# Performance work log

Measured on AMD Instinct MI355X. Metric: run time of the kernel, lower is better.

Reference implementation:

```python
import jax, jax.numpy as jnp
import numpy as np

# ---- layer_param constants (ihmehimmeli alpha-synapse defaults, see shape_source) ----
K_NO_SPIKE = 1000.0
DECAY_RATE = 1.0          # K in exp(K*t)
DECAY_RATE_INV = 1.0
FIRE_THRESHOLD = 1.0
IN_FEATURES = 1024
OUT_FEATURES = 512
N_PULSE = 10
BATCH = 32
MIN_W_ARG = -0.3678794411714423  # -1/e, domain boundary of Lambert W0


def lambertw0(x):
    """Principal branch Lambert W on [-1/e, 0], via Halley iterations."""
    e = jnp.exp(1.0)
    # series init near the branch point, w ~= x for small |x|
    w = jnp.where(x < -0.25,
                  -1.0 + jnp.sqrt(jnp.maximum(2.0 * (1.0 + e * x), 0.0)),
                  x * (1.0 - x))
    def halley(w, _):
        ew = jnp.exp(w)
        f = w * ew - x
        denom = ew * (w + 1.0) - (w + 2.0) * f / (2.0 * (w + 1.0) + 1e-12)
        w = w - f / (denom + 1e-12)
        return w, None
    w, _ = jax.lax.scan(halley, w, None, length=12)
    return w


def _alpha_solve(act, weight):
    """Causal-set cumulative spike-time solve for alpha synapses.
    act: [B,N] input spike times, weight: [O,N].
    V(t) = e^{-K t} (A t - B) with A = sum w e^{K t_i}, B = sum w t_i e^{K t_i};
    threshold crossing: t* = B/A - W0(-theta*K/A * e^{K B/A})/K,
    valid if t* lies between the last included and the next input spike.
    """
    order = jnp.argsort(act, axis=1)                             # [B,N]
    t_s = jnp.take_along_axis(act, order, axis=1)                # sorted spike times
    valid_in = t_s < K_NO_SPIKE
    z = jnp.where(valid_in, jnp.exp(DECAY_RATE * t_s), 0.0)      # exp of valid sorted spikes
    w_s = weight[:, order].transpose(1, 0, 2)                    # [B,O,N] weights in sorted order
    A_c = jnp.cumsum(w_s * z[:, None, :], axis=2)                # causal-set cumulative A
    B_c = jnp.cumsum(w_s * (z * t_s)[:, None, :], axis=2)        # causal-set cumulative B
    A_pos = A_c > 1e-10
    A_safe = jnp.where(A_pos, A_c, 1.0)
    b_over_a = B_c / A_safe
    arg = -FIRE_THRESHOLD * DECAY_RATE / A_safe * jnp.exp(jnp.minimum(DECAY_RATE * b_over_a, 80.0))
    lam_ok = A_pos & (arg >= MIN_W_ARG)
    wl = lambertw0(jnp.clip(arg, MIN_W_ARG, 0.0))
    t_cand = b_over_a - wl * DECAY_RATE_INV
    next_t = jnp.concatenate([t_s[:, 1:], jnp.full_like(t_s[:, :1], K_NO_SPIKE)], axis=1)
    valid = (lam_ok & valid_in[:, None, :]
             & (t_cand >= t_s[:, None, :]) & (t_cand <= next_t[:, None, :]))
    k_star = jnp.argmax(valid, axis=2)                           # first causal set that fires
    spiked = jnp.any(valid, axis=2)
    take = lambda m: jnp.take_along_axis(m, k_star[:, :, None], axis=2)[:, :, 0]
    spike_time = jnp.where(spiked, take(t_cand), K_NO_SPIKE)
    A = jnp.where(spiked, take(A_c), 1.0)
    Bv = jnp.where(spiked, take(B_c), 0.0)
    Wv = jnp.where(spiked, take(wl), 0.0)
    rank = jnp.argsort(order, axis=1)                            # position of each input in sorted order
    causal = rank[:, None, :] <= k_star[:, :, None]              # [B,O,N]
    return spike_time, A, Bv, Wv, causal


def setup_inputs() -> dict:
    key = jax.random.key(0)
    k1, k2 = jax.random.split(key)
    x = jax.random.uniform(k1, (BATCH, IN_FEATURES), dtype=jnp.float32)
    std = float(np.sqrt(2.0 / (IN_FEATURES + OUT_FEATURES)))
    weight = std * 7.0 + std * jax.random.normal(k2, (OUT_FEATURES, IN_FEATURES + N_PULSE), dtype=jnp.float32)
    pulse = jnp.linspace(0.0, 1.0, N_PULSE + 2, dtype=jnp.float32)[1:-1]
    return {"x": x, "weight": weight, "pulse": pulse}


def reference(x, weight, pulse):
    act = jnp.concatenate([x, jnp.broadcast_to(pulse[None, :], (x.shape[0], N_PULSE))], axis=1)
    spike_time, _, _, _, _ = _alpha_solve(act, weight)
    return spike_time
```

## Files before the change

kernel.cpp:

```cpp
#include <hip/hip_runtime.h>
#include <math.h>
#include <limits.h>

#define IN_FEATURES 1024
#define OUT_FEATURES 512
#define N_PULSE 10
#define NCOL 1034
#define BATCH 32
#define MIN_W_ARG -0.3678794411714423

#define NSEG 16
#define SEG 66
#define TBLN 1088

#define OFF_TS  (TBLN * 4)
#define OFF_Z   (TBLN * 8)
#define OFF_ZT  (TBLN * 16)
#define TBL_BYTES (TBLN * 24)

#define PREP_T_BLOCKS 136
#define PREP_BLOCKS (PREP_T_BLOCKS + BATCH)

#define R_KM   0
#define R_KF   4136
#define R_SIDX 8272
#define R_BASE 12408
#define R_RUN  16508
#define R_PS   20604
#define R_BYTES 21632

__global__ __launch_bounds__(256, 1) void prep_kernel(
        const float* __restrict__ w, float* __restrict__ wT,
        const float* __restrict__ x, const float* __restrict__ pulse,
        char* __restrict__ tbl) {
    __shared__ __align__(16) char smem_u[R_BYTES];
    const int tid = threadIdx.x;

    if (blockIdx.x < PREP_T_BLOCKS) {
        float (*tile)[65] = (float (*)[65])smem_u;
        const int n0 = (blockIdx.x % 17) * 64;
        const int o0 = (blockIdx.x / 17) * 64;
        const int tx = tid & 63, ty = tid >> 6;
        #pragma unroll
        for (int r = 0; r < 16; ++r) {
            int ol = r * 4 + ty, n = n0 + tx;
            if (n < NCOL) tile[ol][tx] = w[(o0 + ol) * NCOL + n];
        }
        __syncthreads();
        #pragma unroll
        for (int r = 0; r < 16; ++r) {
            int nl = r * 4 + ty, n = n0 + nl;
            if (n < NCOL) wT[n * OUT_FEATURES + o0 + tx] = tile[tx][nl];
        }
    } else {
        unsigned*  km   = (unsigned*)(smem_u + R_KM);
        float*     kf   = (float*)(smem_u + R_KF);
        int*       sidx = (int*)(smem_u + R_SIDX);
        int*       base = (int*)(smem_u + R_BASE);
        int*       run  = (int*)(smem_u + R_RUN);
        int*       ps   = (int*)(smem_u + R_PS);
        const int b = blockIdx.x - PREP_T_BLOCKS;

        for (int e = tid; e < NCOL; e += 256) {
            float t = (e < IN_FEATURES) ? x[b * IN_FEATURES + e]
                                        : pulse[e - IN_FEATURES];
            kf[e] = t;
            unsigned u = __float_as_uint(t);
            km[e] = (u & 0x80000000u) ? ~u : (u | 0x80000000u);
        }
        for (int i = tid; i < 1024; i += 256) run[i] = 0;
        __syncthreads();

        for (int e = tid; e < NCOL; e += 256) {
            int bk = min(1023, max(0, (int)(kf[e] * 1024.0f)));
            atomicAdd(&run[bk], 1);
        }
        __syncthreads();

        int c4[4], v = 0;
        #pragma unroll
        for (int j = 0; j < 4; ++j) { c4[j] = run[4 * tid + j]; v += c4[j]; }
        ps[tid] = v;
        __syncthreads();
        for (int off = 1; off < 256; off <<= 1) {
            int xv = (tid >= off) ? ps[tid - off] : 0;
            __syncthreads();
            ps[tid] += xv;
            __syncthreads();
        }
        int ex = ps[tid] - v;
        #pragma unroll
        for (int j = 0; j < 4; ++j) { base[4 * tid + j] = ex; ex += c4[j]; }
        if (tid == 255) base[1024] = ex;
        __syncthreads();
        for (int i = tid; i < 1024; i += 256) run[i] = base[i];
        __syncthreads();

        for (int e = tid; e < NCOL; e += 256) {
            int bk = min(1023, max(0, (int)(kf[e] * 1024.0f)));
            int slot = atomicAdd(&run[bk], 1);
            sidx[slot] = e;
        }
        __syncthreads();

        char* gb = tbl + b * TBL_BYTES;
        int*    ordg = (int*)gb;
        float*  tsg  = (float*)(gb + OFF_TS);
        double* zg   = (double*)(gb + OFF_Z);
        double* ztg  = (double*)(gb + OFF_ZT);

        for (int s = tid; s < NCOL; s += 256) {
            int e = sidx[s];
            float t = kf[e];
            unsigned u = km[e];
            int bk = min(1023, max(0, (int)(t * 1024.0f)));
            int lo = base[bk], hi = base[bk + 1];
            int r = lo;
            for (int j = lo; j < hi; ++j) {
                int ej = sidx[j];
                unsigned uj = km[ej];
                r += (uj < u) || (uj == u && ej < e);
            }
            double zv = exp((double)t);
            ordg[r] = e; tsg[r] = t; zg[r] = zv; ztg[r] = zv * (double)t;
        }
        for (int p = NCOL + tid; p < TBLN; p += 256) {
            ordg[p] = 0; tsg[p] = -1.0f; zg[p] = 0.0; ztg[p] = 0.0;
        }
    }
}

__device__ __forceinline__ double lambertw0(double xx) {
    const double e = 2.718281828459045;
    double w = (xx < -0.25) ? (-1.0 + sqrt(fmax(2.0 * (1.0 + e * xx), 0.0)))
                            : xx * (1.0 - xx);
    #pragma unroll 4
    for (int i = 0; i < 12; ++i) {
        double ew = exp(w);
        double f  = w * ew - xx;
        double denom = ew * (w + 1.0) - (w + 2.0) * f / (2.0 * (w + 1.0) + 1e-12);
        w = w - f / (denom + 1e-12);
    }
    return w;
}

__global__ __launch_bounds__(1024) void solve_kernel(
        const float* __restrict__ wT,
        const char* __restrict__ tbl,
        float* __restrict__ out) {
    __shared__ double segA[NSEG * 64], segB[NSEG * 64];
    __shared__ int    sfk[NSEG * 64];
    __shared__ double sfA[NSEG * 64], sfB[NSEG * 64];

    const int b = blockIdx.x >> 3;
    const int o0 = (blockIdx.x & 7) << 6;
    const int wave = threadIdx.x >> 6;
    const int lane = threadIdx.x & 63;
    const int o = o0 + lane;

    const char* base = tbl + b * TBL_BYTES;
    const int*    ordg = (const int*)base;
    const float*  tsg  = (const float*)(base + OFF_TS);
    const double* zg   = (const double*)(base + OFF_Z);
    const double* ztg  = (const double*)(base + OFF_ZT);

    const int k0 = wave * SEG;

    {
        double a0 = 0.0, a1 = 0.0, b0 = 0.0, b1 = 0.0;
        for (int c = 0; c < SEG; c += 11) {
            float buf[11];
            #pragma unroll
            for (int i = 0; i < 11; ++i) {
                int idx = __builtin_amdgcn_readfirstlane(ordg[k0 + c + i]);
                buf[i] = wT[idx * OUT_FEATURES + o];
            }
            #pragma unroll
            for (int i = 0; i < 11; ++i) {
                double w = (double)buf[i];
                if (i & 1) { a1 = fma(w, zg[k0 + c + i], a1);
                             b1 = fma(w, ztg[k0 + c + i], b1); }
                else       { a0 = fma(w, zg[k0 + c + i], a0);
                             b0 = fma(w, ztg[k0 + c + i], b0); }
            }
        }
        segA[wave * 64 + lane] = a0 + a1;
        segB[wave * 64 + lane] = b0 + b1;
    }
    __syncthreads();

    {
        double A = 0.0, Bv = 0.0;
        for (int s = 0; s < wave; ++s) {
            A  += segA[s * 64 + lane];
            Bv += segB[s * 64 + lane];
        }
        int fk = INT_MAX; double fA = 0.0, fB = 0.0;
        for (int c = 0; c < SEG; c += 11) {
            float buf[11];
            #pragma unroll
            for (int i = 0; i < 11; ++i) {
                int idx = __builtin_amdgcn_readfirstlane(ordg[k0 + c + i]);
                buf[i] = wT[idx * OUT_FEATURES + o];
            }
            #pragma unroll
            for (int i = 0; i < 11; ++i) {
                int k = k0 + c + i;
                double w = (double)buf[i];
                A  = fma(w, zg[k],  A);
                Bv = fma(w, ztg[k], Bv);
                bool fire = (fk == INT_MAX) & (A > 1e-10) &
                            (fma(A, (double)tsg[k + 1], -Bv) >= zg[k + 1]);
                if (fire) { fk = k; fA = A; fB = Bv; }
            }
        }
        sfk[wave * 64 + lane] = fk;
        sfA[wave * 64 + lane] = fA;
        sfB[wave * 64 + lane] = fB;
    }
    __syncthreads();

    if (wave == 0) {
        int gk = INT_MAX; double gA = 0.0, gB = 0.0;
        #pragma unroll
        for (int s = 0; s < NSEG; ++s) {
            int k = sfk[s * 64 + lane];
            if (k < gk) { gk = k; gA = sfA[s * 64 + lane]; gB = sfB[s * 64 + lane]; }
        }
        bool done = (gk < NCOL);

        double AA, BB, tk, tn;
        bool have;
        if (done) {
            AA = gA; BB = gB;
            tk = (double)tsg[gk];
            tn = (double)tsg[gk + 1];
            have = true;
        } else {
            double tA = 0.0, tB = 0.0;
            #pragma unroll
            for (int s = 0; s < NSEG; ++s) { tA += segA[s * 64 + lane]; tB += segB[s * 64 + lane]; }
            AA = tA; BB = tB;
            tk = (double)tsg[NCOL - 1];
            tn = 1000.0;
            have = (AA > 1e-10);
        }

        float result = 1000.0f;
        bool need_fb = false;
        if (have) {
            double boa = BB / AA;
            double arg = -exp(fmin(boa, 80.0)) / AA;
            if (arg >= MIN_W_ARG) {
                double wl = lambertw0(fmin(fmax(arg, MIN_W_ARG), 0.0));
                double tc = boa - wl;
                if (tc >= tk && tc <= tn) result = (float)tc;
                else need_fb = done;
            } else need_fb = done;
        }

        if (__ballot(need_fb) != 0ULL) {
            double A2 = gA, B2 = gB;
            for (int k = gk + 1; k < NCOL && k >= 0; ++k) {
                if (!need_fb) break;
                double w = (double)wT[ordg[k] * OUT_FEATURES + o];
                A2 = fma(w, zg[k], A2);
                B2 = fma(w, ztg[k], B2);
                if (!(A2 > 1e-10)) continue;
                double tkk = (double)tsg[k];
                double tnn = (k == NCOL - 1) ? 1000.0 : (double)tsg[k + 1];
                double boa = B2 / A2;
                double arg = -exp(fmin(boa, 80.0)) / A2;
                if (arg >= MIN_W_ARG) {
                    double wl = lambertw0(fmin(fmax(arg, MIN_W_ARG), 0.0));
                    double tc = boa - wl;
                    if (tc >= tkk && tc <= tnn) { result = (float)tc; need_fb = false; }
                }
            }
        }
        out[b * OUT_FEATURES + o] = result;
    }
}

extern "C" void kernel_launch(void* const* d_in, const int* in_sizes, int n_in,
                              void* d_out, int out_size, void* d_ws, size_t ws_size,
                              hipStream_t stream) {
    const float* x      = (const float*)d_in[0];
    const float* weight = (const float*)d_in[1];
    const float* pulse  = (const float*)d_in[2];
    float* out = (float*)d_out;

    char* ws = (char*)d_ws;
    float* wT = (float*)ws;
    char*  tbl = ws + (size_t)NCOL * OUT_FEATURES * 4;

    hipLaunchKernelGGL(prep_kernel, dim3(PREP_BLOCKS), dim3(256), 0, stream,
                       weight, wT, x, pulse, tbl);
    hipLaunchKernelGGL(solve_kernel, dim3(BATCH * OUT_FEATURES / 64), dim3(1024), 0, stream,
                       wT, tbl, out);
}
```

Baseline: 101.2 us.

## Track potential via recurrence P=sum A*dt instead of separate B accumulation

Replaces the cumulative B sum with a potential-like quantity P updated from A and precomputed spike-time gaps, so the fire test becomes a single compare against a precomputed next-z value. The prep kernel now emits packed (z, dt) pairs and a next-z table, and cross-segment prefix combining accounts for the time gaps. B is rebuilt from P only at the chosen index. This removes one load and the fma on t[k+1] per step, but makes the running sum serially dependent on A and may change floating-point rounding.

```diff
diff --git a/kernel.cpp b/kernel.cpp
--- a/kernel.cpp
+++ b/kernel.cpp
@@ -13,10 +13,12 @@
 #define SEG 66
 #define TBLN 1088
 
-#define OFF_TS  (TBLN * 4)
-#define OFF_Z   (TBLN * 8)
-#define OFF_ZT  (TBLN * 16)
-#define TBL_BYTES (TBLN * 24)
+#define OFF_TS   (TBLN * 4)
+#define OFF_Z    (TBLN * 8)
+#define OFF_ZT   (TBLN * 16)
+#define OFF_ZDT  (TBLN * 24)
+#define OFF_ZF   (TBLN * 40)
+#define TBL_BYTES (TBLN * 48)
 
 #define PREP_T_BLOCKS 136
 #define PREP_BLOCKS (PREP_T_BLOCKS + BATCH)
@@ -127,6 +129,21 @@
         for (int p = NCOL + tid; p < TBLN; p += 256) {
             ordg[p] = 0; tsg[p] = -1.0f; zg[p] = 0.0; ztg[p] = 0.0;
         }
+        __threadfence_block();
+        __syncthreads();
+
+        double2* zdtg = (double2*)(gb + OFF_ZDT);
+        double*  zfg  = (double*)(gb + OFF_ZF);
+        for (int r = tid; r < TBLN; r += 256) {
+            double zr = zg[r];
+            double dt, zf;
+            if (r < NCOL - 1)      { dt = (double)tsg[r + 1] - (double)tsg[r]; zf = zg[r + 1]; }
+            else if (r == NCOL - 1){ dt = 1000.0 - (double)tsg[r];             zf = 1e300; }
+            else                   { dt = 0.0;                                 zf = 1e300; }
+            double2 zd; zd.x = zr; zd.y = dt;
+            zdtg[r] = zd;
+            zfg[r]  = zf;
+        }
     }
 }
 
@@ -148,99 +165,106 @@
         const float* __restrict__ wT,
         const char* __restrict__ tbl,
         float* __restrict__ out) {
-    __shared__ double segA[NSEG * 64], segB[NSEG * 64];
-    __shared__ int    sfk[NSEG * 64];
-    __shared__ double sfA[NSEG * 64], sfB[NSEG * 64];
+    __shared__ double dAx[NSEG * 64], dPx[NSEG * 64];
+    __shared__ int    fkx[NSEG * 64];
+    __shared__ double fAx[NSEG * 64], fPx[NSEG * 64];
+    __shared__ double endA[64], endP[64];
 
     const int b = blockIdx.x >> 3;
     const int o0 = (blockIdx.x & 7) << 6;
-    const int wave = threadIdx.x >> 6;
-    const int lane = threadIdx.x & 63;
+    const int tid = threadIdx.x;
+    const int waveu = __builtin_amdgcn_readfirstlane(tid >> 6);
+    const int lane = tid & 63;
     const int o = o0 + lane;
 
     const char* base = tbl + b * TBL_BYTES;
-    const int*    ordg = (const int*)base;
-    const float*  tsg  = (const float*)(base + OFF_TS);
-    const double* zg   = (const double*)(base + OFF_Z);
-    const double* ztg  = (const double*)(base + OFF_ZT);
-
-    const int k0 = wave * SEG;
+    const int*     ordg = (const int*)base;
+    const float*   tsg  = (const float*)(base + OFF_TS);
+    const double*  zg   = (const double*)(base + OFF_Z);
+    const double*  ztg  = (const double*)(base + OFF_ZT);
+    const double2* zdtg = (const double2*)(base + OFF_ZDT);
+    const double*  zfg  = (const double*)(base + OFF_ZF);
+
+    const int k0 = waveu * SEG;
 
     {
-        double a0 = 0.0, a1 = 0.0, b0 = 0.0, b1 = 0.0;
+        double a = 0.0, p = 0.0;
         for (int c = 0; c < SEG; c += 11) {
-            float buf[11];
-            #pragma unroll
-            for (int i = 0; i < 11; ++i) {
-                int idx = __builtin_amdgcn_readfirstlane(ordg[k0 + c + i]);
-                buf[i] = wT[idx * OUT_FEATURES + o];
-            }
+            int so[11]; float buf[11]; double zc[11], dtc[11];
+            #pragma unroll
+            for (int i = 0; i < 11; ++i) so[i] = ordg[k0 + c + i];
+            #pragma unroll
+            for (int i = 0; i < 11; ++i) buf[i] = wT[so[i] * OUT_FEATURES + o];
+            #pragma unroll
+            for (int i = 0; i < 11; ++i) { double2 zd = zdtg[k0 + c + i];
+                                           zc[i] = zd.x; dtc[i] = zd.y; }
             #pragma unroll
             for (int i = 0; i < 11; ++i) {
                 double w = (double)buf[i];
-                if (i & 1) { a1 = fma(w, zg[k0 + c + i], a1);
-                             b1 = fma(w, ztg[k0 + c + i], b1); }
-                else       { a0 = fma(w, zg[k0 + c + i], a0);
-                             b0 = fma(w, ztg[k0 + c + i], b0); }
+                a = fma(w, zc[i], a);
+                p = fma(a, dtc[i], p);
             }
         }
-        segA[wave * 64 + lane] = a0 + a1;
-        segB[wave * 64 + lane] = b0 + b1;
+        dAx[waveu * 64 + lane] = a;
+        dPx[waveu * 64 + lane] = p;
     }
     __syncthreads();
 
     {
-        double A = 0.0, Bv = 0.0;
-        for (int s = 0; s < wave; ++s) {
-            A  += segA[s * 64 + lane];
-            Bv += segB[s * 64 + lane];
-        }
-        int fk = INT_MAX; double fA = 0.0, fB = 0.0;
+        double A = 0.0, P = 0.0;
+        for (int s = 0; s < waveu; ++s) {
+            double dT = (double)tsg[(s + 1) * SEG] - (double)tsg[s * SEG];
+            P += dPx[s * 64 + lane] + A * dT;
+            A += dAx[s * 64 + lane];
+        }
+        int fk = INT_MAX; double fA = 0.0, fP = 0.0;
         for (int c = 0; c < SEG; c += 11) {
-            float buf[11];
+            int so[11]; float buf[11]; double zc[11], dtc[11], zfc[11];
+            #pragma unroll
+            for (int i = 0; i < 11; ++i) so[i] = ordg[k0 + c + i];
+            #pragma unroll
+            for (int i = 0; i < 11; ++i) buf[i] = wT[so[i] * OUT_FEATURES + o];
+            #pragma unroll
+            for (int i = 0; i < 11; ++i) { double2 zd = zdtg[k0 + c + i];
+                                           zc[i] = zd.x; dtc[i] = zd.y; }
+            #pragma unroll
+            for (int i = 0; i < 11; ++i) zfc[i] = zfg[k0 + c + i];
             #pragma unroll
             for (int i = 0; i < 11; ++i) {
-                int idx = __builtin_amdgcn_readfirstlane(ordg[k0 + c + i]);
-                buf[i] = wT[idx * OUT_FEATURES + o];
+                double w = (double)buf[i];
+                A = fma(w, zc[i], A);
+                P = fma(A, dtc[i], P);
+                bool fire = (fk == INT_MAX) & (A > 1e-10) & (P >= zfc[i]);
+                if (fire) { fk = k0 + c + i; fA = A; fP = P; }
             }
-            #pragma unroll
-            for (int i = 0; i < 11; ++i) {
-                int k = k0 + c + i;
-                double w = (double)buf[i];
-                A  = fma(w, zg[k],  A);
-                Bv = fma(w, ztg[k], Bv);
-                bool fire = (fk == INT_MAX) & (A > 1e-10) &
-                            (fma(A, (double)tsg[k + 1], -Bv) >= zg[k + 1]);
-                if (fire) { fk = k; fA = A; fB = Bv; }
-            }
-        }
-        sfk[wave * 64 + lane] = fk;
-        sfA[wave * 64 + lane] = fA;
-        sfB[wave * 64 + lane] = fB;
+        }
+        fkx[waveu * 64 + lane] = fk;
+        fAx[waveu * 64 + lane] = fA;
+        fPx[waveu * 64 + lane] = fP;
+        if (waveu == NSEG - 1) { endA[lane] = A; endP[lane] = P; }
     }
     __syncthreads();
 
-    if (wave == 0) {
-        int gk = INT_MAX; double gA = 0.0, gB = 0.0;
+    if (waveu == 0) {
+        int gk = INT_MAX; double gA = 0.0, gP = 0.0;
         #pragma unroll
         for (int s = 0; s < NSEG; ++s) {
-            int k = sfk[s * 64 + lane];
-            if (k < gk) { gk = k; gA = sfA[s * 64 + lane]; gB = sfB[s * 64 + lane]; }
+            int k = fkx[s * 64 + lane];
+            if (k < gk) { gk = k; gA = fAx[s * 64 + lane]; gP = fPx[s * 64 + lane]; }
         }
         bool done = (gk < NCOL);
 
         double AA, BB, tk, tn;
         bool have;
         if (done) {
-            AA = gA; BB = gB;
+            AA = gA;
             tk = (double)tsg[gk];
             tn = (double)tsg[gk + 1];
+            BB = fma(AA, tn, -gP);
             have = true;
         } else {
-            double tA = 0.0, tB = 0.0;
-            #pragma unroll
-            for (int s = 0; s < NSEG; ++s) { tA += segA[s * 64 + lane]; tB += segB[s * 64 + lane]; }
-            AA = tA; BB = tB;
+            AA = endA[lane];
+            BB = fma(AA, 1000.0, -endP[lane]);
             tk = (double)tsg[NCOL - 1];
             tn = 1000.0;
             have = (AA > 1e-10);
@@ -260,7 +284,7 @@
         }
 
         if (__ballot(need_fb) != 0ULL) {
-            double A2 = gA, B2 = gB;
+            double A2 = gA, B2 = fma(gA, (double)tsg[gk + 1], -gP);
             for (int k = gk + 1; k < NCOL && k >= 0; ++k) {
                 if (!need_fb) break;
                 double w = (double)wT[ordg[k] * OUT_FEATURES + o];
```

Result: faster. 89.84 us (-11.3%).
